# Performance work log

Measured on AMD Instinct MI355X. Metric: run time of the kernel, lower is better.

The kernel has to match this reference:

```python
import jax, jax.numpy as jnp
import numpy as np

B, T, D, H, F = 2, 2048, 2048, 16, 8192
DH = D // H  # 128
EPS = 1e-6   # flax LayerNorm default


def _layernorm(x, scale, bias):
    mu = jnp.mean(x, axis=-1, keepdims=True)
    var = jnp.mean(jnp.square(x - mu), axis=-1, keepdims=True)
    return (x - mu) * jax.lax.rsqrt(var + EPS) * scale + bias


def setup_inputs() -> dict:
    key = jax.random.key(0)
    ks = jax.random.split(key, 8)
    w = 0.02
    return {
        "x": jax.random.normal(ks[0], (B, T, D), jnp.float32),
        "ln1_scale": jnp.ones((D,), jnp.float32),
        "ln1_bias": jnp.zeros((D,), jnp.float32),
        "w_qkv": jax.random.normal(ks[1], (D, 3 * D), jnp.float32) * w,
        "b_qkv": jnp.zeros((3 * D,), jnp.float32),
        "ln2_scale": jnp.ones((D,), jnp.float32),
        "ln2_bias": jnp.zeros((D,), jnp.float32),
        "w1": jax.random.normal(ks[2], (D, F), jnp.float32) * w,
        "b1": jnp.zeros((F,), jnp.float32),
        "w2": jax.random.normal(ks[3], (F, D), jnp.float32) * w,
        "b2": jnp.zeros((D,), jnp.float32),
    }


def reference(x, ln1_scale, ln1_bias, w_qkv, b_qkv, ln2_scale, ln2_bias, w1, b1, w2, b2):
    # --- pre-LN causal self-attention (training=False -> dropout = identity) ---
    r = _layernorm(x, ln1_scale, ln1_bias)
    qkv = r @ w_qkv + b_qkv                       # [B,T,3D]
    q, k, v = jnp.split(qkv, 3, axis=-1)
    q = q.reshape(B, T, H, DH)
    k = k.reshape(B, T, H, DH)
    v = v.reshape(B, T, H, DH)
    attn = jnp.einsum('bthd,bThd->bhtT', q, k) / jnp.sqrt(jnp.float32(DH))
    causal = jnp.tril(jnp.ones((T, T), bool))
    attn = jnp.where(causal, attn, -jnp.inf)
    attn = jax.nn.softmax(attn, axis=-1)
    out = jnp.einsum('bhtT,bThd->bthd', attn, v).reshape(B, T, D)
    # NOTE: original module has no output projection after attention.
    x = x + out
    # --- MLP block ---
    r = _layernorm(x, ln2_scale, ln2_bias)
    h = jax.nn.gelu(r @ w1 + b1, approximate=True)  # flax nn.gelu default
    x = x + (h @ w2 + b2)
    return x
```

## Files before the change

kernel.cpp:

```cpp
#include <hip/hip_runtime.h>
#include <hip/hip_bf16.h>
#include <stdint.h>
#include <stddef.h>

using bf16_t = __hip_bfloat16;
typedef __attribute__((ext_vector_type(8))) short short8;
typedef __attribute__((ext_vector_type(4))) float f32x4;

__device__ __forceinline__ void gload_lds16(const void* g, void* l) {
  __builtin_amdgcn_global_load_lds((const __attribute__((address_space(1))) void*)g,
                                   (__attribute__((address_space(3))) void*)l,
                                   16, 0, 0);
}

__global__ __launch_bounds__(256) void k_transpose_cvt(const float* __restrict__ in,
                                                       bf16_t* __restrict__ out,
                                                       int K, int N) {
  __shared__ float tile[64][65];
  int n0 = blockIdx.x * 64, k0 = blockIdx.y * 64;
  int t = threadIdx.x;
#pragma unroll
  for (int i = 0; i < 16; ++i) {
    int idx = t + i * 256;
    int kk = idx >> 6, nn = idx & 63;
    tile[kk][nn] = in[(size_t)(k0 + kk) * N + n0 + nn];
  }
  __syncthreads();
#pragma unroll
  for (int i = 0; i < 16; ++i) {
    int idx = t + i * 256;
    int nn = idx >> 6, kk = idx & 63;
    out[(size_t)(n0 + nn) * K + k0 + kk] = __float2bfloat16(tile[kk][nn]);
  }
}

__global__ __launch_bounds__(256) void k_layernorm(const float* __restrict__ x,
                                                   const float* __restrict__ gam,
                                                   const float* __restrict__ bet,
                                                   bf16_t* __restrict__ out) {
  int row = blockIdx.x, t = threadIdx.x;
  const float4* xr = (const float4*)(x + (size_t)row * 2048);
  float4 a = xr[t], b = xr[t + 256];
  float s  = a.x + a.y + a.z + a.w + b.x + b.y + b.z + b.w;
  float s2 = a.x*a.x + a.y*a.y + a.z*a.z + a.w*a.w
           + b.x*b.x + b.y*b.y + b.z*b.z + b.w*b.w;
#pragma unroll
  for (int off = 32; off >= 1; off >>= 1) {
    s  += __shfl_xor(s, off);
    s2 += __shfl_xor(s2, off);
  }
  __shared__ float red[8];
  if ((t & 63) == 0) { red[t >> 6] = s; red[4 + (t >> 6)] = s2; }
  __syncthreads();
  float S  = red[0] + red[1] + red[2] + red[3];
  float S2 = red[4] + red[5] + red[6] + red[7];
  float mu = S * (1.0f / 2048.0f);
  float var = S2 * (1.0f / 2048.0f) - mu * mu;
  float rstd = rsqrtf(var + 1e-6f);
  const float4* gv = (const float4*)gam;
  const float4* bv = (const float4*)bet;
  float4 g1 = gv[t], g2 = gv[t + 256], c1 = bv[t], c2 = bv[t + 256];
  bf16_t* orow = out + (size_t)row * 2048;
  orow[4*t + 0]    = __float2bfloat16((a.x - mu) * rstd * g1.x + c1.x);
  orow[4*t + 1]    = __float2bfloat16((a.y - mu) * rstd * g1.y + c1.y);
  orow[4*t + 2]    = __float2bfloat16((a.z - mu) * rstd * g1.z + c1.z);
  orow[4*t + 3]    = __float2bfloat16((a.w - mu) * rstd * g1.w + c1.w);
  orow[1024 + 4*t + 0] = __float2bfloat16((b.x - mu) * rstd * g2.x + c2.x);
  orow[1024 + 4*t + 1] = __float2bfloat16((b.y - mu) * rstd * g2.y + c2.y);
  orow[1024 + 4*t + 2] = __float2bfloat16((b.z - mu) * rstd * g2.z + c2.z);
  orow[1024 + 4*t + 3] = __float2bfloat16((b.w - mu) * rstd * g2.w + c2.w);
}

template <int EPI>
__global__ __launch_bounds__(256, 2) void k_gemm3(const bf16_t* __restrict__ A,
                                                  const bf16_t* __restrict__ Bt,
                                                  const float* __restrict__ bias,
                                                  bf16_t* __restrict__ Cb,
                                                  float* __restrict__ Cf,
                                                  int Ndim, int LDA, int LDB,
                                                  int Kdim, int nkch) {
  __shared__ __align__(16) bf16_t Abuf[2][256 * 32];
  __shared__ __align__(16) bf16_t Bbuf[2][128 * 32];
  int nwg = gridDim.x;
  int orig = blockIdx.x;
  int wg = (orig & 7) * (nwg >> 3) + (orig >> 3);
  int bpc = nwg / nkch;
  int chunk = wg / bpc;
  int rem = wg - chunk * bpc;
  int m0 = (rem & 15) * 256;
  int n0 = (rem >> 4) * 128;
  int tid = threadIdx.x;
  int w = tid >> 6, lane = tid & 63;
  int lr = lane & 15, lk = lane >> 4;
  int wr = w >> 1, wc = w & 1;
  const bf16_t* Ag = A + (size_t)m0 * LDA + (size_t)chunk * Kdim;
  const bf16_t* Bg = Bt + (size_t)n0 * LDB + (size_t)chunk * Kdim;

  f32x4 acc[8][4];
#pragma unroll
  for (int i = 0; i < 8; ++i)
#pragma unroll
    for (int j = 0; j < 4; ++j) acc[i][j] = (f32x4){0.f, 0.f, 0.f, 0.f};
  short8 af[8], bq[4];

  auto stage = [&](int buf, int kt) {
#pragma unroll
    for (int l = 0; l < 4; ++l) {
      int o = l * 256 + tid;
      int row = o >> 2, c = o & 3;
      gload_lds16(Ag + (size_t)row * LDA + kt * 32 + ((c ^ ((row >> 1) & 3)) << 3),
                  &Abuf[buf][o * 8]);
    }
#pragma unroll
    for (int l = 0; l < 2; ++l) {
      int o = l * 256 + tid;
      int row = o >> 2, c = o & 3;
      gload_lds16(Bg + (size_t)row * LDB + kt * 32 + ((c ^ ((row >> 1) & 3)) << 3),
                  &Bbuf[buf][o * 8]);
    }
  };
  auto readfr = [&](int buf) {
#pragma unroll
    for (int mf = 0; mf < 8; ++mf) {
      int row = wr * 128 + mf * 16 + lr;
      int ch = lk ^ ((row >> 1) & 3);
      af[mf] = *(const short8*)&Abuf[buf][row * 32 + ch * 8];
    }
#pragma unroll
    for (int nf = 0; nf < 4; ++nf) {
      int row = wc * 64 + nf * 16 + lr;
      int ch = lk ^ ((row >> 1) & 3);
      bq[nf] = *(const short8*)&Bbuf[buf][row * 32 + ch * 8];
    }
  };
  auto mmac = [&]() {
#pragma unroll
    for (int mf = 0; mf < 8; ++mf)
#pragma unroll
      for (int nf = 0; nf < 4; ++nf)
        acc[mf][nf] = __builtin_amdgcn_mfma_f32_16x16x32_bf16(af[mf], bq[nf], acc[mf][nf], 0, 0, 0);
  };

  const int NT = Kdim >> 5;
  stage(0, 0);
  asm volatile("s_waitcnt vmcnt(0)" ::: "memory");
  asm volatile("s_barrier" ::: "memory");
  for (int t = 0; t < NT - 1; ++t) {
    stage((t & 1) ^ 1, t + 1);
    readfr(t & 1);
    asm volatile("s_waitcnt lgkmcnt(0)" ::: "memory");
    __builtin_amdgcn_sched_barrier(0);
    __builtin_amdgcn_s_setprio(1);
    mmac();
    __builtin_amdgcn_s_setprio(0);
    asm volatile("s_waitcnt vmcnt(0)" ::: "memory");
    asm volatile("s_barrier" ::: "memory");
  }
  readfr((NT - 1) & 1);
  asm volatile("s_waitcnt lgkmcnt(0)" ::: "memory");
  __builtin_amdgcn_sched_barrier(0);
  mmac();

#pragma unroll
  for (int mf = 0; mf < 8; ++mf) {
#pragma unroll
    for (int nf = 0; nf < 4; ++nf) {
#pragma unroll
      for (int r = 0; r < 4; ++r) {
        int rw = m0 + wr * 128 + mf * 16 + lk * 4 + r;
        int cl = n0 + wc * 64 + nf * 16 + lr;
        float v = acc[mf][nf][r];
        size_t gi = (size_t)rw * Ndim + cl;
        if (EPI == 0) {
          Cb[gi] = __float2bfloat16(v + bias[cl]);
        } else if (EPI == 1) {
          float vv = v + bias[cl];
          float u = vv * (vv * vv * 0.044715f + 1.0f) * 0.7978845608028654f;
          float gl = 0.5f * vv * (1.0f + tanhf(u));
          Cb[gi] = __float2bfloat16(gl);
        } else {
          Cf[(size_t)chunk * 4096 * Ndim + gi] = v;
        }
      }
    }
  }
}

__global__ __launch_bounds__(256) void k_reduce(const float* __restrict__ P,
                                                const float* __restrict__ b2,
                                                float* __restrict__ out) {
  int i = blockIdx.x * 1024 + threadIdx.x * 4;
  float4 p0 = *(const float4*)(P + i);
  float4 p1 = *(const float4*)(P + 8388608 + i);
  float4 bb = *(const float4*)(b2 + (i & 2047));
  float4 o  = *(float4*)(out + i);
  o.x += bb.x + p0.x + p1.x;
  o.y += bb.y + p0.y + p1.y;
  o.z += bb.z + p0.z + p1.z;
  o.w += bb.w + p0.w + p1.w;
  *(float4*)(out + i) = o;
}

__global__ __launch_bounds__(256) void k_transpose_v(const bf16_t* __restrict__ qkv,
                                                     bf16_t* __restrict__ vT) {
  __shared__ bf16_t tile[64][72];
  int bid = blockIdx.x;
  int tt = bid & 31;
  int dt = (bid >> 5) & 1;
  int h  = (bid >> 6) & 15;
  int b  = bid >> 10;
  int t0 = tt * 64, d0 = dt * 64;
  int t = threadIdx.x;
  const bf16_t* src = qkv + (size_t)(b * 2048) * 6144 + 4096 + h * 128;
#pragma unroll
  for (int i = 0; i < 16; ++i) {
    int idx = t + i * 256;
    int rr = idx >> 6, cc = idx & 63;
    tile[rr][cc] = src[(size_t)(t0 + rr) * 6144 + d0 + cc];
  }
  __syncthreads();
  bf16_t* dst = vT + (size_t)(b * 16 + h) * 128 * 2048;
#pragma unroll
  for (int i = 0; i < 16; ++i) {
    int idx = t + i * 256;
    int rr = idx >> 6, cc = idx & 63;
    dst[(size_t)(d0 + rr) * 2048 + t0 + cc] = tile[cc][rr];
  }
}

__global__ __launch_bounds__(256, 2) void k_attn(const bf16_t* __restrict__ qkv,
                                                 const bf16_t* __restrict__ vT,
                                                 const float* __restrict__ x,
                                                 float* __restrict__ out) {
  __shared__ __align__(16) bf16_t Pl[4][32][40];
  int j = blockIdx.x;
  int bh = j & 31;
  int cq = j >> 5;
  int b = bh >> 4, h = bh & 15;
  int w = threadIdx.x >> 6, lane = threadIdx.x & 63;
  int lr = lane & 15, lk = lane >> 4;
  int c = (w == 0) ? cq : (w == 1) ? (63 - cq) : (w == 2) ? (31 - cq) : (32 + cq);
  int q0 = c * 32;
  const bf16_t* qb = qkv + (size_t)(b * 2048) * 6144 + h * 128;
  const bf16_t* kb = qb + 2048;
  const bf16_t* vb = vT + (size_t)(b * 16 + h) * 128 * 2048;
  short8 qf[2][4];
#pragma unroll
  for (int qg = 0; qg < 2; ++qg)
#pragma unroll
    for (int d4 = 0; d4 < 4; ++d4)
      qf[qg][d4] = *(const short8*)(qb + (size_t)(q0 + qg * 16 + lr) * 6144 + d4 * 32 + lk * 8);
  float m[2][4], l[2][4];
#pragma unroll
  for (int qg = 0; qg < 2; ++qg)
#pragma unroll
    for (int r = 0; r < 4; ++r) { m[qg][r] = -1e30f; l[qg][r] = 0.f; }
  f32x4 o[2][8] = {};
  int nkt = c + 1;
  const float sc = 0.08838834764831845f;
  for (int kt = 0; kt < nkt; ++kt) {
    int tk0 = kt * 32;
    short8 vf[8];
#pragma unroll
    for (int d8 = 0; d8 < 8; ++d8)
      vf[d8] = *(const short8*)(vb + (size_t)(d8 * 16 + lr) * 2048 + tk0 + lk * 8);
    short8 kf[2][4];
#pragma unroll
    for (int nt = 0; nt < 2; ++nt)
#pragma unroll
      for (int d4 = 0; d4 < 4; ++d4)
        kf[nt][d4] = *(const short8*)(kb + (size_t)(tk0 + nt * 16 + lr) * 6144 + d4 * 32 + lk * 8);
    f32x4 s[2][2] = {};
#pragma unroll
    for (int d4 = 0; d4 < 4; ++d4)
#pragma unroll
      for (int qg = 0; qg < 2; ++qg)
#pragma unroll
        for (int nt = 0; nt < 2; ++nt)
          s[qg][nt] = __builtin_amdgcn_mfma_f32_16x16x32_bf16(qf[qg][d4], kf[nt][d4], s[qg][nt], 0, 0, 0);
#pragma unroll
    for (int qg = 0; qg < 2; ++qg) {
      float sv[2][4], mt[4];
#pragma unroll
      for (int r = 0; r < 4; ++r) {
        int qr = q0 + qg * 16 + lk * 4 + r;
#pragma unroll
        for (int nt = 0; nt < 2; ++nt) {
          float v = s[qg][nt][r] * sc;
          int kc = tk0 + nt * 16 + lr;
          sv[nt][r] = (kc > qr) ? -1e30f : v;
        }
        mt[r] = fmaxf(sv[0][r], sv[1][r]);
      }
#pragma unroll
      for (int off = 1; off < 16; off <<= 1)
#pragma unroll
        for (int r = 0; r < 4; ++r) mt[r] = fmaxf(mt[r], __shfl_xor(mt[r], off));
      float alpha[4], rs[4];
#pragma unroll
      for (int r = 0; r < 4; ++r) {
        float mn = fmaxf(m[qg][r], mt[r]);
        alpha[r] = __expf(m[qg][r] - mn);
        m[qg][r] = mn;
      }
#pragma unroll
      for (int r = 0; r < 4; ++r) {
        float p0 = __expf(sv[0][r] - m[qg][r]);
        float p1 = __expf(sv[1][r] - m[qg][r]);
        rs[r] = p0 + p1;
        Pl[w][qg * 16 + lk * 4 + r][lr]      = __float2bfloat16(p0);
        Pl[w][qg * 16 + lk * 4 + r][16 + lr] = __float2bfloat16(p1);
      }
#pragma unroll
      for (int off = 1; off < 16; off <<= 1)
#pragma unroll
        for (int r = 0; r < 4; ++r) rs[r] += __shfl_xor(rs[r], off);
#pragma unroll
      for (int r = 0; r < 4; ++r) l[qg][r] = l[qg][r] * alpha[r] + rs[r];
#pragma unroll
      for (int d8 = 0; d8 < 8; ++d8)
#pragma unroll
        for (int r = 0; r < 4; ++r) o[qg][d8][r] *= alpha[r];
    }
    asm volatile("s_waitcnt lgkmcnt(0)" ::: "memory");
    short8 pf[2];
#pragma unroll
    for (int qg = 0; qg < 2; ++qg)
      pf[qg] = *(const short8*)(&Pl[w][qg * 16 + lr][lk * 8]);
#pragma unroll
    for (int d8 = 0; d8 < 8; ++d8)
#pragma unroll
      for (int qg = 0; qg < 2; ++qg)
        o[qg][d8] = __builtin_amdgcn_mfma_f32_16x16x32_bf16(pf[qg], vf[d8], o[qg][d8], 0, 0, 0);
  }
#pragma unroll
  for (int qg = 0; qg < 2; ++qg)
#pragma unroll
    for (int d8 = 0; d8 < 8; ++d8)
#pragma unroll
      for (int r = 0; r < 4; ++r) {
        int qr = q0 + qg * 16 + lk * 4 + r;
        int cl = h * 128 + d8 * 16 + lr;
        size_t gi = (size_t)(b * 2048 + qr) * 2048 + cl;
        out[gi] = x[gi] + o[qg][d8][r] / l[qg][r];
      }
}

extern "C" void kernel_launch(void* const* d_in, const int* in_sizes, int n_in,
                              void* d_out, int out_size, void* d_ws, size_t ws_size,
                              hipStream_t stream) {
  const float* x    = (const float*)d_in[0];
  const float* ln1s = (const float*)d_in[1];
  const float* ln1b = (const float*)d_in[2];
  const float* wqkv = (const float*)d_in[3];
  const float* bqkv = (const float*)d_in[4];
  const float* ln2s = (const float*)d_in[5];
  const float* ln2b = (const float*)d_in[6];
  const float* w1   = (const float*)d_in[7];
  const float* b1   = (const float*)d_in[8];
  const float* w2   = (const float*)d_in[9];
  const float* b2   = (const float*)d_in[10];
  float* out = (float*)d_out;
  char* ws = (char*)d_ws;

  bf16_t* r     = (bf16_t*)(ws + 0);
  bf16_t* vT    = (bf16_t*)(ws + 0);
  float*  part  = (float*)(ws + 0);
  bf16_t* qkv   = (bf16_t*)(ws + 16777216);
  bf16_t* w1T   = (bf16_t*)(ws + 67108864);
  bf16_t* w2T   = (bf16_t*)(ws + 100663296);
  bf16_t* h     = (bf16_t*)(ws + 134217728);
  bf16_t* wqkvT = (bf16_t*)(ws + 134217728);

  k_transpose_cvt<<<dim3(96, 32),  256, 0, stream>>>(wqkv, wqkvT, 2048, 6144);
  k_transpose_cvt<<<dim3(128, 32), 256, 0, stream>>>(w1,   w1T,   2048, 8192);
  k_transpose_cvt<<<dim3(32, 128), 256, 0, stream>>>(w2,   w2T,   8192, 2048);
  k_layernorm<<<4096, 256, 0, stream>>>(x, ln1s, ln1b, r);
  k_gemm3<0><<<768, 256, 0, stream>>>(r, wqkvT, bqkv, qkv, nullptr, 6144, 2048, 2048, 2048, 1);
  k_transpose_v<<<2048, 256, 0, stream>>>(qkv, vT);
  k_attn<<<512, 256, 0, stream>>>(qkv, vT, x, out);
  k_layernorm<<<4096, 256, 0, stream>>>(out, ln2s, ln2b, r);
  k_gemm3<1><<<1024, 256, 0, stream>>>(r, w1T, b1, h, nullptr, 8192, 2048, 2048, 2048, 1);
  k_gemm3<3><<<512, 256, 0, stream>>>(h, w2T, nullptr, nullptr, part, 2048, 8192, 8192, 4096, 2);
  k_reduce<<<8192, 256, 0, stream>>>(part, b2, out);
}
```

Measured before the change: 763.4 us.

## Triple-buffer A tiles in GEMM with precomputed addresses and deeper prefetch

Reworks the GEMM main loop so A tiles are triple-buffered and B tiles double-buffered in one 64KB LDS block. Loads for the next tile can stay in flight across the barrier, with a partial vmcnt wait instead of a full drain. Global and LDS addresses are precomputed into pointer and offset registers to cut per-iteration address arithmetic. LDS use rises from 48KB to 64KB, which may limit occupancy at 2 blocks per CU, and uses more registers.

```diff
diff --git a/kernel.cpp b/kernel.cpp
--- a/kernel.cpp
+++ b/kernel.cpp
@@ -72,15 +72,14 @@
 }
 
 template <int EPI>
-__global__ __launch_bounds__(256, 2) void k_gemm3(const bf16_t* __restrict__ A,
+__global__ __launch_bounds__(256, 2) void k_gemm4(const bf16_t* __restrict__ A,
                                                   const bf16_t* __restrict__ Bt,
                                                   const float* __restrict__ bias,
                                                   bf16_t* __restrict__ Cb,
                                                   float* __restrict__ Cf,
                                                   int Ndim, int LDA, int LDB,
                                                   int Kdim, int nkch) {
-  __shared__ __align__(16) bf16_t Abuf[2][256 * 32];
-  __shared__ __align__(16) bf16_t Bbuf[2][128 * 32];
+  __shared__ __align__(16) char lds[65536];
   int nwg = gridDim.x;
   int orig = blockIdx.x;
   int wg = (orig & 7) * (nwg >> 3) + (orig >> 3);
@@ -93,8 +92,25 @@
   int w = tid >> 6, lane = tid & 63;
   int lr = lane & 15, lk = lane >> 4;
   int wr = w >> 1, wc = w & 1;
+
+  int srow = tid >> 2;
+  int scol = ((tid & 3) ^ ((tid >> 3) & 3)) << 3;
   const bf16_t* Ag = A + (size_t)m0 * LDA + (size_t)chunk * Kdim;
   const bf16_t* Bg = Bt + (size_t)n0 * LDB + (size_t)chunk * Kdim;
+  const bf16_t* pA0 = Ag + (size_t)(srow)       * LDA + scol;
+  const bf16_t* pA1 = Ag + (size_t)(srow + 64)  * LDA + scol;
+  const bf16_t* pA2 = Ag + (size_t)(srow + 128) * LDA + scol;
+  const bf16_t* pA3 = Ag + (size_t)(srow + 192) * LDA + scol;
+  const bf16_t* pB0 = Bg + (size_t)(srow)       * LDB + scol;
+  const bf16_t* pB1 = Bg + (size_t)(srow + 64)  * LDB + scol;
+  int dst = tid * 16;
+
+  int ch = (lk ^ ((lr >> 1) & 3)) * 16;
+  int aoff[8], boff[4];
+#pragma unroll
+  for (int mf = 0; mf < 8; ++mf) aoff[mf] = (wr * 128 + mf * 16 + lr) * 64 + ch;
+#pragma unroll
+  for (int nf = 0; nf < 4; ++nf) boff[nf] = 49152 + (wc * 64 + nf * 16 + lr) * 64 + ch;
 
   f32x4 acc[8][4];
 #pragma unroll
@@ -103,63 +119,78 @@
     for (int j = 0; j < 4; ++j) acc[i][j] = (f32x4){0.f, 0.f, 0.f, 0.f};
   short8 af[8], bq[4];
 
-  auto stage = [&](int buf, int kt) {
-#pragma unroll
-    for (int l = 0; l < 4; ++l) {
-      int o = l * 256 + tid;
-      int row = o >> 2, c = o & 3;
-      gload_lds16(Ag + (size_t)row * LDA + kt * 32 + ((c ^ ((row >> 1) & 3)) << 3),
-                  &Abuf[buf][o * 8]);
-    }
-#pragma unroll
-    for (int l = 0; l < 2; ++l) {
-      int o = l * 256 + tid;
-      int row = o >> 2, c = o & 3;
-      gload_lds16(Bg + (size_t)row * LDB + kt * 32 + ((c ^ ((row >> 1) & 3)) << 3),
-                  &Bbuf[buf][o * 8]);
-    }
-  };
-  auto readfr = [&](int buf) {
-#pragma unroll
-    for (int mf = 0; mf < 8; ++mf) {
-      int row = wr * 128 + mf * 16 + lr;
-      int ch = lk ^ ((row >> 1) & 3);
-      af[mf] = *(const short8*)&Abuf[buf][row * 32 + ch * 8];
-    }
-#pragma unroll
-    for (int nf = 0; nf < 4; ++nf) {
-      int row = wc * 64 + nf * 16 + lr;
-      int ch = lk ^ ((row >> 1) & 3);
-      bq[nf] = *(const short8*)&Bbuf[buf][row * 32 + ch * 8];
-    }
-  };
-  auto mmac = [&]() {
-#pragma unroll
-    for (int mf = 0; mf < 8; ++mf)
-#pragma unroll
-      for (int nf = 0; nf < 4; ++nf)
-        acc[mf][nf] = __builtin_amdgcn_mfma_f32_16x16x32_bf16(af[mf], bq[nf], acc[mf][nf], 0, 0, 0);
-  };
-
+#define STAGE_A()  do { \
+    gload_lds16(pA0, lds + a_wr + dst);          \
+    gload_lds16(pA1, lds + a_wr + 4096 + dst);   \
+    gload_lds16(pA2, lds + a_wr + 8192 + dst);   \
+    gload_lds16(pA3, lds + a_wr + 12288 + dst);  \
+    pA0 += 32; pA1 += 32; pA2 += 32; pA3 += 32; } while (0)
+#define STAGE_B()  do { \
+    gload_lds16(pB0, lds + 49152 + b_wr + dst);        \
+    gload_lds16(pB1, lds + 49152 + b_wr + 4096 + dst); \
+    pB0 += 32; pB1 += 32; } while (0)
+#define READ_FR()  do { \
+    _Pragma("unroll") for (int mf = 0; mf < 8; ++mf) \
+      af[mf] = *(const short8*)(lds + a_rd + aoff[mf]); \
+    _Pragma("unroll") for (int nf = 0; nf < 4; ++nf) \
+      bq[nf] = *(const short8*)(lds + b_rd + boff[nf]); } while (0)
+#define MMAC()  do { \
+    _Pragma("unroll") for (int mf = 0; mf < 8; ++mf) \
+      _Pragma("unroll") for (int nf = 0; nf < 4; ++nf) \
+        acc[mf][nf] = __builtin_amdgcn_mfma_f32_16x16x32_bf16(af[mf], bq[nf], acc[mf][nf], 0, 0, 0); } while (0)
+#define LGKM0()  do { asm volatile("s_waitcnt lgkmcnt(0)" ::: "memory"); __builtin_amdgcn_sched_barrier(0); } while (0)
+#define VM(N)    asm volatile("s_waitcnt vmcnt(%0)" :: "i"(N) : "memory")
+#define BARRIER() asm volatile("s_barrier" ::: "memory")
+
+  int a_rd = 0, a_wr = 32768;
+  int b_rd = 0, b_wr = 8192;
   const int NT = Kdim >> 5;
-  stage(0, 0);
-  asm volatile("s_waitcnt vmcnt(0)" ::: "memory");
-  asm volatile("s_barrier" ::: "memory");
-  for (int t = 0; t < NT - 1; ++t) {
-    stage((t & 1) ^ 1, t + 1);
-    readfr(t & 1);
-    asm volatile("s_waitcnt lgkmcnt(0)" ::: "memory");
-    __builtin_amdgcn_sched_barrier(0);
+
+  { int sva = a_wr, svb = b_wr;
+    a_wr = 0;     STAGE_A();
+    b_wr = 0;     STAGE_B();
+    a_wr = 16384; STAGE_A();
+    a_wr = sva;   b_wr = svb; }
+  VM(4);
+  BARRIER();
+
+  for (int t = 0; t < NT - 2; ++t) {
+    STAGE_B();
+    STAGE_A();
+    READ_FR();
+    LGKM0();
     __builtin_amdgcn_s_setprio(1);
-    mmac();
+    MMAC();
     __builtin_amdgcn_s_setprio(0);
-    asm volatile("s_waitcnt vmcnt(0)" ::: "memory");
-    asm volatile("s_barrier" ::: "memory");
-  }
-  readfr((NT - 1) & 1);
-  asm volatile("s_waitcnt lgkmcnt(0)" ::: "memory");
-  __builtin_amdgcn_sched_barrier(0);
-  mmac();
+    VM(4);
+    BARRIER();
+    int fr = a_rd; a_rd = (a_rd == 32768) ? 0 : a_rd + 16384; a_wr = fr;
+    fr = b_rd; b_rd = b_wr; b_wr = fr;
+  }
+  {
+    STAGE_B();
+    READ_FR();
+    LGKM0();
+    __builtin_amdgcn_s_setprio(1);
+    MMAC();
+    __builtin_amdgcn_s_setprio(0);
+    VM(0);
+    BARRIER();
+    a_rd = (a_rd == 32768) ? 0 : a_rd + 16384;
+    b_rd = b_wr;
+  }
+  {
+    READ_FR();
+    LGKM0();
+    MMAC();
+  }
+#undef STAGE_A
+#undef STAGE_B
+#undef READ_FR
+#undef MMAC
+#undef LGKM0
+#undef VM
+#undef BARRIER
 
 #pragma unroll
   for (int mf = 0; mf < 8; ++mf) {
@@ -376,11 +407,11 @@
   k_transpose_cvt<<<dim3(128, 32), 256, 0, stream>>>(w1,   w1T,   2048, 8192);
   k_transpose_cvt<<<dim3(32, 128), 256, 0, stream>>>(w2,   w2T,   8192, 2048);
   k_layernorm<<<4096, 256, 0, stream>>>(x, ln1s, ln1b, r);
-  k_gemm3<0><<<768, 256, 0, stream>>>(r, wqkvT, bqkv, qkv, nullptr, 6144, 2048, 2048, 2048, 1);
+  k_gemm4<0><<<768, 256, 0, stream>>>(r, wqkvT, bqkv, qkv, nullptr, 6144, 2048, 2048, 2048, 1);
   k_transpose_v<<<2048, 256, 0, stream>>>(qkv, vT);
   k_attn<<<512, 256, 0, stream>>>(qkv, vT, x, out);
   k_layernorm<<<4096, 256, 0, stream>>>(out, ln2s, ln2b, r);
-  k_gemm3<1><<<1024, 256, 0, stream>>>(r, w1T, b1, h, nullptr, 8192, 2048, 2048, 2048, 1);
-  k_gemm3<3><<<512, 256, 0, stream>>>(h, w2T, nullptr, nullptr, part, 2048, 8192, 8192, 4096, 2);
+  k_gemm4<1><<<1024, 256, 0, stream>>>(r, w1T, b1, h, nullptr, 8192, 2048, 2048, 2048, 1);
+  k_gemm4<3><<<512, 256, 0, stream>>>(h, w2T, nullptr, nullptr, part, 2048, 8192, 8192, 4096, 2);
   k_reduce<<<8192, 256, 0, stream>>>(part, b2, out);
 }
```

Result: faster. 685.3 us (-10.2%).
